# Optimization experiments

Measured on AMD Instinct MI355X. Metric: run time of the kernel, lower is better.

Reference implementation:

```python
import jax, jax.numpy as jnp
import numpy as np

B, T, I, H = 64, 512, 512, 512

def setup_inputs() -> dict:
    key = jax.random.key(0)
    ks = jax.random.split(key, 13)
    s = 0.02
    return {
        'inputs': jax.random.normal(ks[0], (B, T, I), dtype=jnp.float32),
        'W_i': jax.random.normal(ks[1], (I, H), dtype=jnp.float32) * s,
        'W_f': jax.random.normal(ks[2], (I, H), dtype=jnp.float32) * s,
        'W_o': jax.random.normal(ks[3], (I, H), dtype=jnp.float32) * s,
        'W_c': jax.random.normal(ks[4], (I, H), dtype=jnp.float32) * s,
        'U_i': jax.random.normal(ks[5], (H, H), dtype=jnp.float32) * s,
        'U_f': jax.random.normal(ks[6], (H, H), dtype=jnp.float32) * s,
        'U_o': jax.random.normal(ks[7], (H, H), dtype=jnp.float32) * s,
        'U_c': jax.random.normal(ks[8], (H, H), dtype=jnp.float32) * s,
        'b_i': jax.random.normal(ks[9], (1, H), dtype=jnp.float32) * s,
        'b_f': jax.random.normal(ks[10], (1, H), dtype=jnp.float32) * s,
        'b_o': jax.random.normal(ks[11], (1, H), dtype=jnp.float32) * s,
        'b_c': jax.random.normal(ks[12], (1, H), dtype=jnp.float32) * s,
    }

def reference(inputs, W_i, W_f, W_o, W_c, U_i, U_f, U_o, U_c, b_i, b_f, b_o, b_c):
    batch = inputs.shape[0]
    hidden = U_i.shape[0]
    # Precompute input projections for all 4 gates in one fused GEMM: [T, B, 4H]
    W = jnp.concatenate([W_i, W_f, W_o, W_c], axis=1)          # [I, 4H]
    b = jnp.concatenate([b_i, b_f, b_o, b_c], axis=1)          # [1, 4H]
    U = jnp.concatenate([U_i, U_f, U_o, U_c], axis=1)          # [H, 4H]
    x_proj = jnp.einsum('bti,ig->tbg', inputs, W) + b          # [T, B, 4H]

    def step(carry, xg):
        h, c = carry
        g = xg + h @ U                                          # [B, 4H]
        i_g = jax.nn.sigmoid(g[:, 0*hidden:1*hidden])
        f_g = jax.nn.sigmoid(g[:, 1*hidden:2*hidden])
        o_g = jax.nn.sigmoid(g[:, 2*hidden:3*hidden])
        c_t = jnp.tanh(g[:, 3*hidden:4*hidden])
        c = f_g * c + i_g * c_t
        h = o_g * jnp.tanh(c)
        return (h, c), None

    h0 = jnp.zeros((batch, hidden), dtype=inputs.dtype)
    c0 = jnp.zeros((batch, hidden), dtype=inputs.dtype)
    (h, c), _ = jax.lax.scan(step, (h0, c0), x_proj)
    return h
```

## Files before the change

### kernel.cpp

```cpp
#include <hip/hip_runtime.h>
#include <hip/hip_bf16.h>
#include <cstdint>


typedef __bf16 bf16;
typedef __bf16 bf16x8 __attribute__((ext_vector_type(8)));
typedef float floatx4 __attribute__((ext_vector_type(4)));
typedef uint64_t u64;
typedef uint32_t u32;

#define T_STEPS 512

#define XP_OFF     0ull
#define XBF_OFF    134217728ull
#define WCT_OFF    167772160ull
#define USW_OFF    169869312ull
#define BCAT_OFF   171966464ull
#define HBUF_OFF   171974656ull

__device__ inline u32 pack_bf16x2(float a, float b) {
    union { __bf16 h[2]; u32 u; } cv;
    cv.h[0] = (__bf16)a; cv.h[1] = (__bf16)b;
    return cv.u;
}
__device__ inline float bf_lo(u32 w) { return __builtin_bit_cast(float, w << 16); }
__device__ inline float bf_hi(u32 w) { return __builtin_bit_cast(float, w & 0xffff0000u); }

__device__ inline void lgkm_barrier() {
    __atomic_signal_fence(__ATOMIC_SEQ_CST);
    __builtin_amdgcn_s_waitcnt(0xc07f);
    __builtin_amdgcn_s_barrier();
    __atomic_signal_fence(__ATOMIC_SEQ_CST);
}

__device__ inline void wave_lds_fence() {
    __atomic_signal_fence(__ATOMIC_SEQ_CST);
    __builtin_amdgcn_s_waitcnt(0xc07f);
    __builtin_amdgcn_sched_barrier(0);
    __atomic_signal_fence(__ATOMIC_SEQ_CST);
}

__global__ void k0a_convert(const float* __restrict__ in, bf16* __restrict__ xbf) {
    int o = blockIdx.x * 256 + threadIdx.x;
    int k = o & 511;
    int r = o >> 9;
    int t = r >> 6, b = r & 63;
    xbf[o] = (bf16)in[(b * 512 + t) * 512 + k];
}

__global__ void k0b_wcat(const float* __restrict__ Wi, const float* __restrict__ Wf,
                         const float* __restrict__ Wo, const float* __restrict__ Wc,
                         const float* __restrict__ bi, const float* __restrict__ bfv,
                         const float* __restrict__ bo, const float* __restrict__ bc,
                         bf16* __restrict__ wct, float* __restrict__ bcat) {
    int o = blockIdx.x * 256 + threadIdx.x;
    int k = o & 511;
    int c = o >> 9;
    int h = c >> 2, g = c & 3;
    const float* W = (g == 0) ? Wi : (g == 1) ? Wf : (g == 2) ? Wo : Wc;
    wct[o] = (bf16)W[k * 512 + h];
    if (o < 2048) {
        int hh = o >> 2, gg = o & 3;
        const float* bv = (gg == 0) ? bi : (gg == 1) ? bfv : (gg == 2) ? bo : bc;
        bcat[o] = bv[hh];
    }
}

__global__ void k0c_uswz(const float* __restrict__ Ui, const float* __restrict__ Uf,
                         const float* __restrict__ Uo, const float* __restrict__ Uc,
                         bf16* __restrict__ usw) {
    int o = blockIdx.x * 256 + threadIdx.x;
    int e  = o & 7;
    int l  = (o >> 3) & 63;
    int ks = (o >> 9) & 15;
    int nt = (o >> 13) & 1;
    int w  = (o >> 14) & 3;
    int s  = o >> 16;
    int k = ks * 32 + (l >> 4) * 8 + e;
    int col_local = (2 * w + nt) * 16 + (l & 15);
    int h = s * 32 + (col_local >> 2);
    int g = col_local & 3;
    const float* U = (g == 0) ? Ui : (g == 1) ? Uf : (g == 2) ? Uo : Uc;
    usw[o] = (bf16)U[k * 512 + h];
}

__launch_bounds__(256, 2)
__global__ void k1_gemm(const bf16* __restrict__ xbf, const bf16* __restrict__ wct,
                        const float* __restrict__ bcat, bf16* __restrict__ xp) {
    __shared__ bf16 As[128 * 40];
    __shared__ bf16 Bs[128 * 40];
    int tid = threadIdx.x;
    int wid = tid >> 6, lane = tid & 63;
    int q = lane >> 4, m = lane & 15;
    int wr = wid >> 1, wc = wid & 1;
    int br = blockIdx.x & 255, bc = blockIdx.x >> 8;

    floatx4 acc[4][4] = {};

    for (int kk = 0; kk < 16; ++kk) {
        #pragma unroll
        for (int cc = 0; cc < 2; ++cc) {
            int ch = tid + cc * 256;
            int row = ch >> 2, part = ch & 3;
            bf16x8 va = *(const bf16x8*)&xbf[(br * 128 + row) * 512 + kk * 32 + part * 8];
            bf16x8 vb = *(const bf16x8*)&wct[(bc * 128 + row) * 512 + kk * 32 + part * 8];
            *(bf16x8*)&As[row * 40 + part * 8] = va;
            *(bf16x8*)&Bs[row * 40 + part * 8] = vb;
        }
        __syncthreads();
        bf16x8 af[4], bfr[4];
        #pragma unroll
        for (int i = 0; i < 4; ++i) {
            af[i]  = *(const bf16x8*)&As[(wr * 64 + i * 16 + m) * 40 + q * 8];
            bfr[i] = *(const bf16x8*)&Bs[(wc * 64 + i * 16 + m) * 40 + q * 8];
        }
        #pragma unroll
        for (int mt = 0; mt < 4; ++mt)
            #pragma unroll
            for (int nt = 0; nt < 4; ++nt)
                acc[mt][nt] = __builtin_amdgcn_mfma_f32_16x16x32_bf16(
                    af[mt], bfr[nt], acc[mt][nt], 0, 0, 0);
        __syncthreads();
    }
    float bias[4];
    #pragma unroll
    for (int nt = 0; nt < 4; ++nt) bias[nt] = bcat[bc * 128 + wc * 64 + nt * 16 + m];
    #pragma unroll
    for (int mt = 0; mt < 4; ++mt) {
        #pragma unroll
        for (int nt = 0; nt < 4; ++nt) {
            u32 p0 = pack_bf16x2(acc[mt][nt][0] + bias[nt], acc[mt][nt][1] + bias[nt]);
            u32 p1 = pack_bf16x2(acc[mt][nt][2] + bias[nt], acc[mt][nt][3] + bias[nt]);
            size_t idx = (((((size_t)(br * 2 + wr) * 4 + mt) * 16 + bc) * 8
                           + wc * 4 + nt) * 64 + lane) * 4;
            uint2 v; v.x = p0; v.y = p1;
            *(uint2*)&xp[idx] = v;
        }
    }
}

__launch_bounds__(256, 1)
__global__ void k2_rec(const bf16* __restrict__ xp, const bf16* __restrict__ usw,
                       u64* __restrict__ hbuf, float* __restrict__ out) {
    __shared__ u32 h_sh[2][16 * 256];
    __shared__ float g_slab[4][16 * 36];

    int tid = threadIdx.x;
    int wid = tid >> 6, lane = tid & 63;
    int q = lane >> 4, m = lane & 15;
    int bg = blockIdx.x & 3, s = blockIdx.x >> 2;

    bf16x8 bfr[2][16];
    {
        const bf16x8* base = (const bf16x8*)usw;
        #pragma unroll
        for (int nt = 0; nt < 2; ++nt)
            #pragma unroll
            for (int ks = 0; ks < 16; ++ks)
                bfr[nt][ks] = base[(((s * 4 + wid) * 2 + nt) * 16 + ks) * 64 + lane];
    }

    int r2 = lane >> 2;
    int kk2 = lane & 3;
    float cs0 = 0.f, cs1 = 0.f;

    int wc = tid >> 2, wk = tid & 3;

    float* gs = &g_slab[wid][0];

    uint2 vx0, vx1;
    {
        size_t b0 = ((((size_t)bg * 16 + s) * 8 + wid * 2) * 64 + lane) * 4;
        vx0 = *(const uint2*)&xp[b0];
        vx1 = *(const uint2*)&xp[b0 + 256];
    }

    for (int t = 0; t < T_STEPS; ++t) {
        floatx4 acc[2];

        acc[0][0] = bf_lo(vx0.x); acc[0][1] = bf_hi(vx0.x);
        acc[0][2] = bf_lo(vx0.y); acc[0][3] = bf_hi(vx0.y);
        acc[1][0] = bf_lo(vx1.x); acc[1][1] = bf_hi(vx1.x);
        acc[1][2] = bf_lo(vx1.y); acc[1][3] = bf_hi(vx1.y);

        if (t > 0) {
            __atomic_signal_fence(__ATOMIC_SEQ_CST);
            __builtin_amdgcn_s_sleep(8);
            __atomic_signal_fence(__ATOMIC_SEQ_CST);

            const u64* rb = hbuf + ((size_t)((t - 1) & 1) * 4 + bg) * 4096;
            u32 tg = (u32)t;
            u64 w[16];
            #pragma unroll
            for (int i = 0; i < 16; ++i)
                w[i] = __hip_atomic_load(rb + tid + 256 * i, __ATOMIC_RELAXED,
                                         __HIP_MEMORY_SCOPE_AGENT);
            for (;;) {
                bool ok = true;
                #pragma unroll
                for (int i = 0; i < 16; ++i) ok &= ((u32)(w[i] >> 32) == tg);
                if (ok) break;
                #pragma unroll
                for (int i = 0; i < 16; ++i)
                    w[i] = __hip_atomic_load(rb + tid + 256 * i, __ATOMIC_RELAXED,
                                             __HIP_MEMORY_SCOPE_AGENT);
            }
            u32* hp = &h_sh[(t & 1) ^ 1][0];
            #pragma unroll
            for (int i = 0; i < 16; ++i)
                hp[i * 256 + ((wc ^ (i & 7)) << 2) + wk] = (u32)w[i];
            lgkm_barrier();
            const bf16* hbs = (const bf16*)hp;
            floatx4 accb0 = {}, accb1 = {};
            #pragma unroll
            for (int ks = 0; ks < 8; ++ks) {
                bf16x8 af = *(const bf16x8*)&hbs[m * 512 + (((4 * ks + q) ^ (m & 7)) << 3)];
                acc[0] = __builtin_amdgcn_mfma_f32_16x16x32_bf16(af, bfr[0][ks], acc[0], 0, 0, 0);
                acc[1] = __builtin_amdgcn_mfma_f32_16x16x32_bf16(af, bfr[1][ks], acc[1], 0, 0, 0);
            }
            #pragma unroll
            for (int ks = 8; ks < 16; ++ks) {
                bf16x8 af = *(const bf16x8*)&hbs[m * 512 + (((4 * ks + q) ^ (m & 7)) << 3)];
                accb0 = __builtin_amdgcn_mfma_f32_16x16x32_bf16(af, bfr[0][ks], accb0, 0, 0, 0);
                accb1 = __builtin_amdgcn_mfma_f32_16x16x32_bf16(af, bfr[1][ks], accb1, 0, 0, 0);
            }
            acc[0] += accb0;
            acc[1] += accb1;
        }

        if (t + 1 < T_STEPS) {
            size_t b0 = (((((size_t)(t + 1) * 4 + bg) * 16 + s) * 8 + wid * 2) * 64 + lane) * 4;
            vx0 = *(const uint2*)&xp[b0];
            vx1 = *(const uint2*)&xp[b0 + 256];
        }

        #pragma unroll
        for (int nt = 0; nt < 2; ++nt)
            #pragma unroll
            for (int rr = 0; rr < 4; ++rr)
                gs[(q * 4 + rr) * 36 + nt * 16 + m] = acc[nt][rr];
        wave_lds_fence();

        floatx4 ga = *(const floatx4*)&gs[r2 * 36 + kk2 * 8];
        floatx4 gb = *(const floatx4*)&gs[r2 * 36 + kk2 * 8 + 4];
        float h0, h1;
        {
            float ig = 1.f / (1.f + __expf(-ga[0]));
            float fg = 1.f / (1.f + __expf(-ga[1]));
            float og = 1.f / (1.f + __expf(-ga[2]));
            float th = 1.f - 2.f / (__expf(2.f * ga[3]) + 1.f);
            cs0 = fg * cs0 + ig * th;
            h0 = og * (1.f - 2.f / (__expf(2.f * cs0) + 1.f));
        }
        {
            float ig = 1.f / (1.f + __expf(-gb[0]));
            float fg = 1.f / (1.f + __expf(-gb[1]));
            float og = 1.f / (1.f + __expf(-gb[2]));
            float th = 1.f - 2.f / (__expf(2.f * gb[3]) + 1.f);
            cs1 = fg * cs1 + ig * th;
            h1 = og * (1.f - 2.f / (__expf(2.f * cs1) + 1.f));
        }
        u64 word = ((u64)(u32)(t + 1) << 32) | (u64)pack_bf16x2(h0, h1);
        (void)__hip_atomic_exchange(
            hbuf + (((size_t)(t & 1) * 4 + bg) * 16 + r2) * 256
                 + s * 16 + wid * 4 + kk2,
            word, __ATOMIC_RELAXED, __HIP_MEMORY_SCOPE_AGENT);
        if (t == T_STEPS - 1) {
            int u0 = s * 32 + wid * 8 + kk2 * 2;
            out[(bg * 16 + r2) * 512 + u0]     = h0;
            out[(bg * 16 + r2) * 512 + u0 + 1] = h1;
        }
    }
}

extern "C" void kernel_launch(void* const* d_in, const int* in_sizes, int n_in,
                              void* d_out, int out_size, void* d_ws, size_t ws_size,
                              hipStream_t stream) {
    const float* inp = (const float*)d_in[0];
    const float* Wi  = (const float*)d_in[1];
    const float* Wf  = (const float*)d_in[2];
    const float* Wo  = (const float*)d_in[3];
    const float* Wc  = (const float*)d_in[4];
    const float* Ui  = (const float*)d_in[5];
    const float* Uf  = (const float*)d_in[6];
    const float* Uo  = (const float*)d_in[7];
    const float* Uc  = (const float*)d_in[8];
    const float* bi  = (const float*)d_in[9];
    const float* bfv = (const float*)d_in[10];
    const float* bo  = (const float*)d_in[11];
    const float* bc  = (const float*)d_in[12];

    char* ws = (char*)d_ws;
    bf16*  xp    = (bf16*)(ws + XP_OFF);
    bf16*  xbf   = (bf16*)(ws + XBF_OFF);
    bf16*  wct   = (bf16*)(ws + WCT_OFF);
    bf16*  usw   = (bf16*)(ws + USW_OFF);
    float* bcat  = (float*)(ws + BCAT_OFF);
    u64*   hbuf  = (u64*)(ws + HBUF_OFF);

    k0a_convert<<<65536, 256, 0, stream>>>(inp, xbf);
    k0b_wcat<<<4096, 256, 0, stream>>>(Wi, Wf, Wo, Wc, bi, bfv, bo, bc, wct, bcat);
    k0c_uswz<<<4096, 256, 0, stream>>>(Ui, Uf, Uo, Uc, usw);
    k1_gemm<<<4096, 256, 0, stream>>>(xbf, wct, bcat, xp);
    k2_rec<<<64, 256, 0, stream>>>(xp, usw, hbuf, (float*)d_out);
}
```

Before: 1.478 ms.

## Use nontemporal loads/stores, fast rcp activations, selective polling, plain atomic store

Several micro-optimizations land at once. Streaming input conversion, xp stores and xp loads now use nontemporal hints. The gate activations use hardware reciprocal instead of IEEE division. The spin-wait reloads only words whose tag is still stale. The h publish becomes a relaxed atomic store instead of an exchange. These changes target per-step latency in the serial recurrence and cache pollution, at the cost of slightly lower activation precision and a data-dependent branch in the poll loop.

```diff
diff --git a/kernel.cpp b/kernel.cpp
--- a/kernel.cpp
+++ b/kernel.cpp
@@ -26,6 +26,13 @@
 __device__ inline float bf_lo(u32 w) { return __builtin_bit_cast(float, w << 16); }
 __device__ inline float bf_hi(u32 w) { return __builtin_bit_cast(float, w & 0xffff0000u); }
 
+__device__ inline float fast_sigmoid(float x) {
+    return __builtin_amdgcn_rcpf(1.f + __expf(-x));
+}
+__device__ inline float fast_tanh(float x) {
+    return 1.f - 2.f * __builtin_amdgcn_rcpf(__expf(2.f * x) + 1.f);
+}
+
 __device__ inline void lgkm_barrier() {
     __atomic_signal_fence(__ATOMIC_SEQ_CST);
     __builtin_amdgcn_s_waitcnt(0xc07f);
@@ -45,7 +52,8 @@
     int k = o & 511;
     int r = o >> 9;
     int t = r >> 6, b = r & 63;
-    xbf[o] = (bf16)in[(b * 512 + t) * 512 + k];
+    float v = __builtin_nontemporal_load(&in[(b * 512 + t) * 512 + k]);
+    xbf[o] = (bf16)v;
 }
 
 __global__ void k0b_wcat(const float* __restrict__ Wi, const float* __restrict__ Wf,
@@ -133,8 +141,8 @@
             u32 p1 = pack_bf16x2(acc[mt][nt][2] + bias[nt], acc[mt][nt][3] + bias[nt]);
             size_t idx = (((((size_t)(br * 2 + wr) * 4 + mt) * 16 + bc) * 8
                            + wc * 4 + nt) * 64 + lane) * 4;
-            uint2 v; v.x = p0; v.y = p1;
-            *(uint2*)&xp[idx] = v;
+            u64 pv = (u64)p0 | ((u64)p1 << 32);
+            __builtin_nontemporal_store(pv, (u64*)&xp[idx]);
         }
     }
 }
@@ -168,20 +176,24 @@
 
     float* gs = &g_slab[wid][0];
 
-    uint2 vx0, vx1;
+    u64 vx0, vx1;
     {
         size_t b0 = ((((size_t)bg * 16 + s) * 8 + wid * 2) * 64 + lane) * 4;
-        vx0 = *(const uint2*)&xp[b0];
-        vx1 = *(const uint2*)&xp[b0 + 256];
+        vx0 = __builtin_nontemporal_load((const u64*)&xp[b0]);
+        vx1 = __builtin_nontemporal_load((const u64*)&xp[b0 + 256]);
     }
 
     for (int t = 0; t < T_STEPS; ++t) {
         floatx4 acc[2];
 
-        acc[0][0] = bf_lo(vx0.x); acc[0][1] = bf_hi(vx0.x);
-        acc[0][2] = bf_lo(vx0.y); acc[0][3] = bf_hi(vx0.y);
-        acc[1][0] = bf_lo(vx1.x); acc[1][1] = bf_hi(vx1.x);
-        acc[1][2] = bf_lo(vx1.y); acc[1][3] = bf_hi(vx1.y);
+        {
+            u32 x0 = (u32)vx0, x1 = (u32)(vx0 >> 32);
+            u32 x2 = (u32)vx1, x3 = (u32)(vx1 >> 32);
+            acc[0][0] = bf_lo(x0); acc[0][1] = bf_hi(x0);
+            acc[0][2] = bf_lo(x1); acc[0][3] = bf_hi(x1);
+            acc[1][0] = bf_lo(x2); acc[1][1] = bf_hi(x2);
+            acc[1][2] = bf_lo(x3); acc[1][3] = bf_hi(x3);
+        }
 
         if (t > 0) {
             __atomic_signal_fence(__ATOMIC_SEQ_CST);
@@ -202,8 +214,9 @@
                 if (ok) break;
                 #pragma unroll
                 for (int i = 0; i < 16; ++i)
-                    w[i] = __hip_atomic_load(rb + tid + 256 * i, __ATOMIC_RELAXED,
-                                             __HIP_MEMORY_SCOPE_AGENT);
+                    if ((u32)(w[i] >> 32) != tg)
+                        w[i] = __hip_atomic_load(rb + tid + 256 * i, __ATOMIC_RELAXED,
+                                                 __HIP_MEMORY_SCOPE_AGENT);
             }
             u32* hp = &h_sh[(t & 1) ^ 1][0];
             #pragma unroll
@@ -230,8 +243,8 @@
 
         if (t + 1 < T_STEPS) {
             size_t b0 = (((((size_t)(t + 1) * 4 + bg) * 16 + s) * 8 + wid * 2) * 64 + lane) * 4;
-            vx0 = *(const uint2*)&xp[b0];
-            vx1 = *(const uint2*)&xp[b0 + 256];
+            vx0 = __builtin_nontemporal_load((const u64*)&xp[b0]);
+            vx1 = __builtin_nontemporal_load((const u64*)&xp[b0 + 256]);
         }
 
         #pragma unroll
@@ -245,26 +258,25 @@
         floatx4 gb = *(const floatx4*)&gs[r2 * 36 + kk2 * 8 + 4];
         float h0, h1;
         {
-            float ig = 1.f / (1.f + __expf(-ga[0]));
-            float fg = 1.f / (1.f + __expf(-ga[1]));
-            float og = 1.f / (1.f + __expf(-ga[2]));
-            float th = 1.f - 2.f / (__expf(2.f * ga[3]) + 1.f);
+            float ig = fast_sigmoid(ga[0]);
+            float fg = fast_sigmoid(ga[1]);
+            float og = fast_sigmoid(ga[2]);
+            float th = fast_tanh(ga[3]);
             cs0 = fg * cs0 + ig * th;
-            h0 = og * (1.f - 2.f / (__expf(2.f * cs0) + 1.f));
+            h0 = og * fast_tanh(cs0);
         }
         {
-            float ig = 1.f / (1.f + __expf(-gb[0]));
-            float fg = 1.f / (1.f + __expf(-gb[1]));
-            float og = 1.f / (1.f + __expf(-gb[2]));
-            float th = 1.f - 2.f / (__expf(2.f * gb[3]) + 1.f);
+            float ig = fast_sigmoid(gb[0]);
+            float fg = fast_sigmoid(gb[1]);
+            float og = fast_sigmoid(gb[2]);
+            float th = fast_tanh(gb[3]);
             cs1 = fg * cs1 + ig * th;
-            h1 = og * (1.f - 2.f / (__expf(2.f * cs1) + 1.f));
+            h1 = og * fast_tanh(cs1);
         }
         u64 word = ((u64)(u32)(t + 1) << 32) | (u64)pack_bf16x2(h0, h1);
-        (void)__hip_atomic_exchange(
-            hbuf + (((size_t)(t & 1) * 4 + bg) * 16 + r2) * 256
-                 + s * 16 + wid * 4 + kk2,
-            word, __ATOMIC_RELAXED, __HIP_MEMORY_SCOPE_AGENT);
+        __hip_atomic_store(hbuf + (((size_t)(t & 1) * 4 + bg) * 16 + r2) * 256
+                                + s * 16 + wid * 4 + kk2,
+                           word, __ATOMIC_RELAXED, __HIP_MEMORY_SCOPE_AGENT);
         if (t == T_STEPS - 1) {
             int u0 = s * 32 + wid * 8 + kk2 * 2;
             out[(bg * 16 + r2) * 512 + u0]     = h0;
```

Measured after the change: 1.461 ms. About the same (-1.2%).
